# Optimization experiments

Measured on AMD Instinct MI355X. Metric: run time of the kernel, lower is better.

The kernel has to match this reference:

```python
import jax, jax.numpy as jnp
import numpy as np

TEMPLATE_SZ = 7
MAX_SR = 3


def setup_inputs() -> dict:
    key = jax.random.key(0)
    # image-like values in [0, 255) since the module ends with a uint8 cast
    x = jax.random.uniform(key, (2, 1, 192, 192), dtype=jnp.float32) * 255.0
    return {"inputs": x, "search_range": 3}


def reference(inputs, search_range):
    # Equivalent math to: pad(max_sr) -> unfold(k, pad=k//2) -> unfold(s) ->
    # permute -> slice sub-window -> reshape -> uint8.
    # Both zero-pads commute, so fold them into one pad and gather directly,
    # avoiding the huge duplicated double-im2col intermediate.
    k = TEMPLATE_SZ
    max_sr = MAX_SR
    cv = 2 * search_range + 1          # cost_volume_sz
    offset = max_sr - search_range
    B, C, H, W = inputs.shape          # C == 1 (implied by the torch view)
    pad = max_sr + k // 2              # combined zero padding
    Q = jnp.pad(inputs[:, 0].astype(jnp.float32), ((0, 0), (pad, pad), (pad, pad)))
    r = offset + jnp.arange(cv)        # search offsets within max window
    t = jnp.arange(k)                  # template offsets
    # windows[b,i,j,dy,dx,ty,tx] = Q[b, i + r[dy] + ty, j + r[dx] + tx]
    iy = jnp.arange(H)[:, None, None] + r[None, :, None] + t[None, None, :]  # [H, cv, k]
    jx = jnp.arange(W)[:, None, None] + r[None, :, None] + t[None, None, :]  # [W, cv, k]
    win = Q[:, iy[:, None, :, None, :, None], jx[None, :, None, :, None, :]]  # [B,H,W,cv,cv,k,k]
    return win.reshape(B, H, W, cv * cv, k * k).astype(jnp.uint8)
```

## Files before the change

kernel.cpp:

```cpp
#include <hip/hip_runtime.h>


#define KT 7
#define K2 49
#define MAX_SR 3
#define B_ 2
#define H_ 192
#define W_ 192
#define HW (H_ * W_)
#define PAD 6
#define NT 256
#define NBLOCKS 512
#define WPB (NT / 64)
#define NWAVES (NBLOCKS * WPB)
#define PS 17
#define BUFI 280
#define NGROUPS (B_ * H_ * W_ / 4)
#define TABQ 2560
#define TABN (4 * TABQ)

typedef int vint4 __attribute__((ext_vector_type(4)));

__device__ __forceinline__ int swz(int e) { return e + (e >> 2); }

__device__ __forceinline__ int tab_entry(int jj, int cv, int offset, int d,
                                         int cvmagic) {
    if (jj >= 4 * d) jj = 4 * d - 1;
    int p_in = (jj >= d) + (jj >= 2 * d) + (jj >= 3 * d);
    int j  = jj - p_in * d;
    int rr = j / K2;
    int tt = j - rr * K2;
    int ry = (rr * cvmagic) >> 16;
    int rx = rr - ry * cv;
    int ty = tt / KT;
    int tx = tt - ty * KT;
    int e = (offset + ry + ty) * PS + (offset + rx + tx) + p_in;
    return 4 * swz(e);
}

__global__ __launch_bounds__(256) void tab_kernel(
    int* __restrict__ tab, int cv, int offset, int d, int cvmagic)
{
    int jj = blockIdx.x * 256 + threadIdx.x;
    if (jj < TABN) tab[jj] = tab_entry(jj, cv, offset, d, cvmagic);
}

__global__ __launch_bounds__(NT, 2) void esw_kernel(
    const float* __restrict__ in, int* __restrict__ out,
    const int* __restrict__ tab,
    int cv, int offset, int d, int cvmagic)
{
    __shared__ int patch[WPB][BUFI];

    const int tid  = threadIdx.x;
    const int lane = tid & 63;
    const int wv   = tid >> 6;
    int* const pbuf = patch[wv];
    const char* const pb = (const char*)pbuf;

    const int NR  = (4 * d + 255) >> 8;
    const int wid = blockIdx.x * WPB + wv;

    for (int g = wid; g < NGROUPS; g += NWAVES) {
        const int pix0 = 4 * g;
        const int b   = pix0 / HW;
        const int rem = pix0 - b * HW;
        const int h   = rem / W_;
        const int w   = rem - h * W_;
        #pragma unroll
        for (int k = 0; k < 4; ++k) {
            int e = lane + 64 * k;
            if (e < 13 * 16) {
                int dy = e >> 4, dx = e & 15;
                int y = h + dy - PAD, x = w + dx - PAD;
                int v = 0;
                if ((unsigned)y < (unsigned)H_ && (unsigned)x < (unsigned)W_)
                    v = (int)in[b * HW + y * W_ + x];
                pbuf[swz(dy * PS + dx)] = v;
            }
        }
        asm volatile("s_waitcnt lgkmcnt(0)" ::: "memory");

        int* op = out + g * (4 * d);
        if (tab) {
            vint4 t = *(const vint4*)(tab + 4 * lane);
            for (int r = 0; r < NR; ++r) {
                vint4 tn = *(const vint4*)(tab + 4 * (64 * (r + 1) + lane));
                int q = 64 * r + lane;
                if (q < d) {
                    vint4 v;
                    v.x = *(const int*)(pb + t.x);
                    v.y = *(const int*)(pb + t.y);
                    v.z = *(const int*)(pb + t.z);
                    v.w = *(const int*)(pb + t.w);
                    *(vint4*)(op + 4 * q) = v;
                }
                t = tn;
            }
        } else {
            for (int r = 0; r < NR; ++r) {
                int q = 64 * r + lane;
                if (q < d) {
                    vint4 v;
                    v.x = *(const int*)(pb + tab_entry(4 * q + 0, cv, offset, d, cvmagic));
                    v.y = *(const int*)(pb + tab_entry(4 * q + 1, cv, offset, d, cvmagic));
                    v.z = *(const int*)(pb + tab_entry(4 * q + 2, cv, offset, d, cvmagic));
                    v.w = *(const int*)(pb + tab_entry(4 * q + 3, cv, offset, d, cvmagic));
                    *(vint4*)(op + 4 * q) = v;
                }
            }
        }
        asm volatile("s_waitcnt lgkmcnt(0)" ::: "memory");
    }
}

extern "C" void kernel_launch(void* const* d_in, const int* in_sizes, int n_in,
                              void* d_out, int out_size, void* d_ws, size_t ws_size,
                              hipStream_t stream) {
    const float* in = (const float*)d_in[0];
    int* out = (int*)d_out;

    int cv2 = out_size / (B_ * H_ * W_ * K2);
    int cv = 1;
    while (cv * cv < cv2) ++cv;
    int offset = MAX_SR - (cv - 1) / 2;
    int d = cv2 * K2;
    int cvmagic = 65536 / cv + 1;

    int* tab = (ws_size >= (size_t)(TABN * sizeof(int))) ? (int*)d_ws : nullptr;
    if (tab)
        tab_kernel<<<(TABN + 255) / 256, 256, 0, stream>>>(tab, cv, offset, d,
                                                           cvmagic);
    esw_kernel<<<NBLOCKS, NT, 0, stream>>>(in, out, tab, cv, offset, d, cvmagic);
}
```

Baseline: 693.0 us.

## Process each pixel group with a whole 512-thread block sharing one patch

Work moves from one wavefront per 4-pixel group, with a per-wave LDS patch, to one 512-thread block per group that shares a single patch and synchronises with block barriers. The gather/store loop over the d vec4 outputs is spread across 512 threads and unrolled to a fixed bound of 5 iterations, and the index table grows to cover that stride. The aim is fewer redundant patch loads per block and more store parallelism per group. The cost is two block-wide barriers per iteration, which can stall the waves and reduce overlap between groups.

Result: slower. 715.2 us (+3.2%).

```diff
diff --git a/kernel.cpp b/kernel.cpp
--- a/kernel.cpp
+++ b/kernel.cpp
@@ -9,14 +9,13 @@
 #define W_ 192
 #define HW (H_ * W_)
 #define PAD 6
-#define NT 256
-#define NBLOCKS 512
-#define WPB (NT / 64)
-#define NWAVES (NBLOCKS * WPB)
+#define NT 512
+#define NBLOCKS 256
 #define PS 17
 #define BUFI 280
 #define NGROUPS (B_ * H_ * W_ / 4)
-#define TABQ 2560
+#define NITER (NGROUPS / NBLOCKS)
+#define TABQ 3072
 #define TABN (4 * TABQ)
 
 typedef int vint4 __attribute__((ext_vector_type(4)));
@@ -50,43 +49,43 @@
     const int* __restrict__ tab,
     int cv, int offset, int d, int cvmagic)
 {
-    __shared__ int patch[WPB][BUFI];
+    __shared__ int patch[BUFI];
 
-    const int tid  = threadIdx.x;
-    const int lane = tid & 63;
-    const int wv   = tid >> 6;
-    int* const pbuf = patch[wv];
-    const char* const pb = (const char*)pbuf;
+    const int tid = threadIdx.x;
+    const int bid = blockIdx.x;
+    const char* const pb = (const char*)patch;
 
-    const int NR  = (4 * d + 255) >> 8;
-    const int wid = blockIdx.x * WPB + wv;
+    const int NR = (d + NT - 1) / NT;
 
-    for (int g = wid; g < NGROUPS; g += NWAVES) {
-        const int pix0 = 4 * g;
-        const int b   = pix0 / HW;
-        const int rem = pix0 - b * HW;
-        const int h   = rem / W_;
-        const int w   = rem - h * W_;
-        #pragma unroll
-        for (int k = 0; k < 4; ++k) {
-            int e = lane + 64 * k;
-            if (e < 13 * 16) {
-                int dy = e >> 4, dx = e & 15;
-                int y = h + dy - PAD, x = w + dx - PAD;
-                int v = 0;
-                if ((unsigned)y < (unsigned)H_ && (unsigned)x < (unsigned)W_)
-                    v = (int)in[b * HW + y * W_ + x];
-                pbuf[swz(dy * PS + dx)] = v;
-            }
+    for (int it = 0; it < NITER; ++it) {
+        const int g = it * NBLOCKS + bid;
+
+        if (tid < 13 * 16) {
+            int dy = tid >> 4, dx = tid & 15;
+            const int pix0 = 4 * g;
+            const int b   = pix0 / HW;
+            const int rem = pix0 - b * HW;
+            const int h   = rem / W_;
+            const int w   = rem - h * W_;
+            int y = h + dy - PAD, x = w + dx - PAD;
+            int v = 0;
+            if ((unsigned)y < (unsigned)H_ && (unsigned)x < (unsigned)W_)
+                v = (int)in[b * HW + y * W_ + x];
+            patch[swz(dy * PS + dx)] = v;
         }
         asm volatile("s_waitcnt lgkmcnt(0)" ::: "memory");
+        __builtin_amdgcn_sched_barrier(0);
+        __builtin_amdgcn_s_barrier();
+        __builtin_amdgcn_sched_barrier(0);
 
         int* op = out + g * (4 * d);
         if (tab) {
-            vint4 t = *(const vint4*)(tab + 4 * lane);
-            for (int r = 0; r < NR; ++r) {
-                vint4 tn = *(const vint4*)(tab + 4 * (64 * (r + 1) + lane));
-                int q = 64 * r + lane;
+            vint4 t = *(const vint4*)(tab + 4 * tid);
+            #pragma unroll
+            for (int r = 0; r < 5; ++r) {
+                if (r >= NR) break;
+                vint4 tn = *(const vint4*)(tab + 4 * (NT * (r + 1) + tid));
+                int q = NT * r + tid;
                 if (q < d) {
                     vint4 v;
                     v.x = *(const int*)(pb + t.x);
@@ -98,19 +97,18 @@
                 t = tn;
             }
         } else {
-            for (int r = 0; r < NR; ++r) {
-                int q = 64 * r + lane;
-                if (q < d) {
-                    vint4 v;
-                    v.x = *(const int*)(pb + tab_entry(4 * q + 0, cv, offset, d, cvmagic));
-                    v.y = *(const int*)(pb + tab_entry(4 * q + 1, cv, offset, d, cvmagic));
-                    v.z = *(const int*)(pb + tab_entry(4 * q + 2, cv, offset, d, cvmagic));
-                    v.w = *(const int*)(pb + tab_entry(4 * q + 3, cv, offset, d, cvmagic));
-                    *(vint4*)(op + 4 * q) = v;
-                }
+            for (int q = tid; q < d; q += NT) {
+                vint4 v;
+                v.x = *(const int*)(pb + tab_entry(4 * q + 0, cv, offset, d, cvmagic));
+                v.y = *(const int*)(pb + tab_entry(4 * q + 1, cv, offset, d, cvmagic));
+                v.z = *(const int*)(pb + tab_entry(4 * q + 2, cv, offset, d, cvmagic));
+                v.w = *(const int*)(pb + tab_entry(4 * q + 3, cv, offset, d, cvmagic));
+                *(vint4*)(op + 4 * q) = v;
             }
         }
-        asm volatile("s_waitcnt lgkmcnt(0)" ::: "memory");
+        __builtin_amdgcn_sched_barrier(0);
+        __builtin_amdgcn_s_barrier();
+        __builtin_amdgcn_sched_barrier(0);
     }
 }
 
```
